# Kernel tuning notes

Hardware: AMD Instinct MI355X
Metric: run time of the kernel (lower is better)

Reference implementation:

```python
import jax, jax.numpy as jnp
import numpy as np

HIDDEN = 256
HEAD = 256
GAMMA = 0.96875
SCALE_BASE = 512  # default scale_base in the standard XPOS module


def xpos_apply(x, offset=0, downscale=False):
    """xpos rotary embedding. x: (B, S, H) with H even."""
    B, S, H = x.shape
    half = H // 2
    dt = x.dtype
    pos = jnp.arange(offset, offset + S, dtype=dt)  # (S,)
    # per-channel xpos scale: ((2i + 0.4H) / (1.4H)) ** (pos / scale_base)
    base_scale = (jnp.arange(0, H, 2, dtype=dt) + 0.4 * H) / (1.4 * H)  # (half,)
    scale = base_scale[None, :] ** (pos[:, None] / SCALE_BASE)          # (S, half)
    if downscale:
        scale = 1.0 / scale
    inv_freq = 1.0 / (10000.0 ** (jnp.arange(half, dtype=dt) / half))   # (half,)
    sinusoid = pos[:, None] * inv_freq[None, :]                         # (S, half)
    sin = jnp.sin(sinusoid) * scale
    cos = jnp.cos(sinusoid) * scale
    # duplicate-interleave columns to width H
    sin2 = jnp.repeat(sin, 2, axis=-1)  # (S, H)
    cos2 = jnp.repeat(cos, 2, axis=-1)
    # rotate_every_two
    x1 = x[..., 0::2]
    x2 = x[..., 1::2]
    rot = jnp.stack([-x2, x1], axis=-1).reshape(x.shape)
    return x * cos2[None] + rot * sin2[None]


def decay_mask(S, dtype):
    n = jnp.arange(S)
    diff = n[:, None] - n[None, :]
    # gamma^(i-j) for i>=j else 0 (clamp exponent to avoid huge values under the mask)
    D = jnp.where(diff >= 0,
                  jnp.asarray(GAMMA, dtype) ** jnp.maximum(diff, 0).astype(dtype),
                  jnp.zeros((), dtype))
    return D


def setup_inputs() -> dict:
    key = jax.random.key(0)
    k1, k2, k3, k4 = jax.random.split(key, 4)
    B, N, S = 2, 8, 2048
    X = jax.random.normal(k1, (B, N, S, HIDDEN), dtype=jnp.float32)
    # kaiming-uniform-ish init: uniform in [-1/sqrt(fan_in), 1/sqrt(fan_in)]
    bound = 1.0 / np.sqrt(HIDDEN)
    W_Q = jax.random.uniform(k2, (HIDDEN, HEAD), jnp.float32, -bound, bound)
    W_K = jax.random.uniform(k3, (HIDDEN, HEAD), jnp.float32, -bound, bound)
    W_V = jax.random.uniform(k4, (HIDDEN, HEAD), jnp.float32, -bound, bound)
    return {"X": X, "W_Q": W_Q, "W_K": W_K, "W_V": W_V}


def reference(X, W_Q, W_K, W_V):
    B, N, S, H = X.shape
    Q = X @ W_Q  # (B, N, S, head)
    K = X @ W_K
    V = X @ W_V
    hd = Q.shape[-1]
    Q = xpos_apply(Q.reshape(B * N, S, hd)).reshape(B, N, S, hd)
    K = xpos_apply(K.reshape(B * N, S, hd), downscale=True).reshape(B, N, S, hd)
    D = decay_mask(S, X.dtype)  # (S, S)
    scores = jnp.einsum('bnsh,bnth->bnst', Q, K) * D  # (B, N, S, S)
    return scores @ V  # (B, N, S, v_dim)
```

## Files before the change

### kernel.cpp

```cpp
#include <hip/hip_runtime.h>
#include <hip/hip_bf16.h>


#define S_LEN 2048
#define HD 256
#define BN 16

typedef _Float16 half8 __attribute__((ext_vector_type(8)));
typedef _Float16 half4 __attribute__((ext_vector_type(4)));
typedef _Float16 half2v __attribute__((ext_vector_type(2)));
typedef float floatx16 __attribute__((ext_vector_type(16)));

__device__ __forceinline__ void gl_lds16(const void* g, void* l) {
  __builtin_amdgcn_global_load_lds(
      (const __attribute__((address_space(1))) unsigned int*)(unsigned long long)g,
      (__attribute__((address_space(3))) unsigned int*)(unsigned int)(unsigned long long)l,
      16, 0, 0);
}

__global__ __launch_bounds__(256) void prep_kernel(
    const float* __restrict__ WQ, const float* __restrict__ WK,
    const float* __restrict__ WV, _Float16* __restrict__ WT,
    _Float16* __restrict__ TBL) {
  const int b = blockIdx.x;
  const int tid = threadIdx.x;
  if (b < 1024) {
    const int idx = b * 256 + tid;
    const int i2 = idx & 127;
    const int pos = idx >> 7;
    float inv_freq = exp2f(-(float)i2 * (13.287712379549449f / 128.0f));
    float lbase = log2f(((float)(2 * i2) + 102.4f) / 358.4f);
    float ang = (float)pos * inv_freq;
    float sn, cs;
    sincosf(ang, &sn, &cs);
    float scl = exp2f((float)pos * (1.0f / 512.0f) * lbase);
    float rscl = 1.0f / scl;
    half2v tq, tk;
    tq[0] = (_Float16)(cs * scl);  tq[1] = (_Float16)(sn * scl);
    tk[0] = (_Float16)(cs * rscl); tk[1] = (_Float16)(sn * rscl);
    *(half2v*)&TBL[(long)idx * 2] = tq;
    *(half2v*)&TBL[(long)(262144 + idx) * 2] = tk;
    return;
  }
  __shared__ _Float16 trans[64][72];
  const int bb = b - 1024;
  const int w = bb >> 4;
  const int tk = ((bb & 15) & 3) * 64;
  const int tn = ((bb & 15) >> 2) * 64;
  const float* W = (w == 0) ? WQ : (w == 1) ? WK : WV;
#pragma unroll
  for (int u = 0; u < 4; ++u) {
    int idx = u * 256 + tid;
    int k = idx >> 4;
    int nq = (idx & 15) * 4;
    float4 v = *(const float4*)&W[(tk + k) * HD + tn + nq];
    trans[nq + 0][k] = (_Float16)v.x;
    trans[nq + 1][k] = (_Float16)v.y;
    trans[nq + 2][k] = (_Float16)v.z;
    trans[nq + 3][k] = (_Float16)v.w;
  }
  __syncthreads();
#pragma unroll
  for (int u = 0; u < 2; ++u) {
    int idx = u * 256 + tid;
    int n = idx >> 3;
    int kq = (idx & 7) * 8;
    *(uint4*)&WT[((long)w * HD + tn + n) * HD + tk + kq] = *(const uint4*)&trans[n][kq];
  }
}

__global__ __launch_bounds__(256) void gemm_qkv_kernel(
    const float* __restrict__ X, const _Float16* __restrict__ WT,
    const _Float16* __restrict__ TBL,
    _Float16* __restrict__ Q, _Float16* __restrict__ K,
    _Float16* __restrict__ VT) {
  __shared__ __align__(16) unsigned char smem[66560];
  unsigned char* ep = smem + 32768;

  const int tid = threadIdx.x;
  const int lane = tid & 63;
  const int w = tid >> 6;
  const int l31 = lane & 31;
  const int lh = lane >> 5;
  const int m0 = blockIdx.x * 64;
  const int mtile = w & 1;
  const int nhalf = w >> 1;

#pragma unroll
  for (int i = 0; i < 8; ++i) {
    int id = i * 256 + tid;
    int row = id >> 5, c = id & 31;
    int p = c ^ (row & 31);
    const float4* s = (const float4*)&X[(long)(m0 + row) * HD + c * 8];
    float4 v0 = s[0], v1 = s[1];
    half8 h;
    h[0] = (_Float16)v0.x; h[1] = (_Float16)v0.y;
    h[2] = (_Float16)v0.z; h[3] = (_Float16)v0.w;
    h[4] = (_Float16)v1.x; h[5] = (_Float16)v1.y;
    h[6] = (_Float16)v1.z; h[7] = (_Float16)v1.w;
    *(half8*)(smem + row * 512 + p * 16) = h;
  }
  __syncthreads();

  const int bn = m0 >> 11;
  const int srow0 = m0 & (S_LEN - 1);
  const int mrow = mtile * 32 + l31;
  const int nbase = nhalf * 128;

  for (int wsel = 0; wsel < 3; ++wsel) {
    const _Float16* Wb = WT + (long)wsel * HD * HD;
    floatx16 acc[4];
#pragma unroll
    for (int nt = 0; nt < 4; ++nt)
#pragma unroll
      for (int e = 0; e < 16; ++e) acc[nt][e] = 0.f;

    half8 b[5][4];
#pragma unroll
    for (int pk = 0; pk < 5; ++pk)
#pragma unroll
      for (int nt = 0; nt < 4; ++nt)
        b[pk][nt] = *(const half8*)(Wb + (long)(nbase + nt * 32 + l31) * HD +
                                    pk * 16 + lh * 8);
#pragma unroll
    for (int ks16 = 0; ks16 < 16; ++ks16) {
      const int slot = ks16 % 5;
      int p = (ks16 * 2 + lh) ^ l31;
      half8 af = *(const half8*)(smem + mrow * 512 + p * 16);
#pragma unroll
      for (int nt = 0; nt < 4; ++nt)
        acc[nt] = __builtin_amdgcn_mfma_f32_32x32x16_f16(af, b[slot][nt], acc[nt], 0, 0, 0);
      if (ks16 + 5 < 16) {
#pragma unroll
        for (int nt = 0; nt < 4; ++nt)
          b[slot][nt] = *(const half8*)(Wb + (long)(nbase + nt * 32 + l31) * HD +
                                        (ks16 + 5) * 16 + lh * 8);
      }
    }

    if (wsel < 2) {
#pragma unroll
      for (int nt = 0; nt < 4; ++nt) {
        int col = nbase + nt * 32 + l31;
#pragma unroll
        for (int reg = 0; reg < 16; ++reg) {
          int rmap = (reg & 3) + 8 * (reg >> 2) + 4 * lh;
          *(_Float16*)(ep + (mtile * 32 + rmap) * 528 + col * 2) =
              (_Float16)acc[nt][reg];
        }
      }
      __syncthreads();
      _Float16* o = wsel ? K : Q;
      const _Float16* tb_base = TBL + (long)wsel * 2048 * 128 * 2;
#pragma unroll
      for (int u = 0; u < 8; ++u) {
        int id = u * 256 + tid;
        int row = id >> 5;
        int cq = (id & 31) * 8;
        half8 x = *(const half8*)(ep + row * 528 + cq * 2);
        half8 t = *(const half8*)&tb_base[((long)(srow0 + row) * 128 + (cq >> 1)) * 2];
        half8 y;
        y[0] = x[0] * t[0] - x[1] * t[1];
        y[1] = x[1] * t[0] + x[0] * t[1];
        y[2] = x[2] * t[2] - x[3] * t[3];
        y[3] = x[3] * t[2] + x[2] * t[3];
        y[4] = x[4] * t[4] - x[5] * t[5];
        y[5] = x[5] * t[4] + x[4] * t[5];
        y[6] = x[6] * t[6] - x[7] * t[7];
        y[7] = x[7] * t[6] + x[6] * t[7];
        *(half8*)&o[(long)(m0 + row) * HD + cq] = y;
      }
      __syncthreads();
    } else {
      __syncthreads();
      _Float16 (*vt)[72] = (_Float16(*)[72])smem;
#pragma unroll
      for (int nt = 0; nt < 4; ++nt) {
        int h = nbase + nt * 32 + l31;
#pragma unroll
        for (int reg = 0; reg < 16; ++reg) {
          int rmap = (reg & 3) + 8 * (reg >> 2) + 4 * lh;
          vt[h][mtile * 32 + rmap] = (_Float16)acc[nt][reg];
        }
      }
      __syncthreads();
#pragma unroll
      for (int u = 0; u < 8; ++u) {
        int id = u * 256 + tid;
        int h = id >> 3, sj = (id & 7) * 8;
        *(uint4*)&VT[((long)bn * HD + h) * S_LEN + srow0 + sj] = *(const uint4*)&vt[h][sj];
      }
    }
  }
}

__global__ __launch_bounds__(256) void retention_kernel(
    const _Float16* __restrict__ Q, const _Float16* __restrict__ K,
    const _Float16* __restrict__ VT, float* __restrict__ out) {
  __shared__ __align__(16) unsigned char smem[74752];
  unsigned char* ksb = smem;
  unsigned char* vsb = smem + 32768;
  _Float16 (*sc)[72] = (_Float16(*)[72])(smem + 65536);

  const int tid = threadIdx.x;
  const int lane = tid & 63;
  const int w = tid >> 6;
  const int l31 = lane & 31;
  const int lh = lane >> 5;
  const int qtile = w >> 1;
  const int ttile = w & 1;
  const int hhalf = w & 1;

  const int L = blockIdx.x;
  const int head = L & 15;
  const int g4 = L >> 4;
  const int qt = (g4 < 16) ? (31 - g4) : (g4 - 16);
  const int q0 = qt * 64;

  const _Float16* Qh = Q + (long)head * S_LEN * HD;
  const _Float16* Kh = K + (long)head * S_LEN * HD;
  const _Float16* VTh = VT + (long)head * HD * S_LEN;

  half8 qf[16];
  {
    const _Float16* qrow = Qh + (long)(q0 + qtile * 32 + l31) * HD + lh * 8;
#pragma unroll
    for (int ks16 = 0; ks16 < 16; ++ks16)
      qf[ks16] = *(const half8*)(qrow + ks16 * 16);
  }

  floatx16 acc[4];
#pragma unroll
  for (int nt = 0; nt < 4; ++nt)
#pragma unroll
    for (int e = 0; e < 16; ++e) acc[nt][e] = 0.f;

  const float LG = -0.0458036896f;
  float Cg[16];
#pragma unroll
  for (int g = 0; g < 4; ++g)
#pragma unroll
    for (int r = 0; r < 4; ++r) Cg[4 * g + r] = exp2f(-(float)(8 * g + r) * LG);

#define STAGE_K(T0)                                                        \
  {                                                                        \
    _Pragma("unroll") for (int j = 0; j < 8; ++j) {                        \
      int li = w * 8 + j;                                                  \
      int row = li * 2 + lh;                                               \
      int c = l31 ^ (row & 31);                                            \
      gl_lds16(Kh + (long)((T0) + row) * HD + c * 8, ksb + li * 1024);     \
    }                                                                      \
  }
#define STAGE_V(T0)                                                        \
  {                                                                        \
    _Pragma("unroll") for (int j = 0; j < 8; ++j) {                        \
      int li = w * 8 + j;                                                  \
      int row = li * 8 + (lane >> 3);                                      \
      int c = (lane & 7) ^ (row & 7);                                      \
      gl_lds16(VTh + (long)row * S_LEN + (T0) + c * 8, vsb + li * 1024);   \
    }                                                                      \
  }

  STAGE_K(0);
  STAGE_V(0);

  for (int kt = 0; kt <= qt; ++kt) {
    const int t0 = kt * 64;
    asm volatile("s_waitcnt vmcnt(0)" ::: "memory");
    __syncthreads();

    floatx16 s;
#pragma unroll
    for (int e = 0; e < 16; ++e) s[e] = 0.f;
    {
      const unsigned char* kbase = ksb + (ttile * 32 + l31) * 512;
#pragma unroll
      for (int ks16 = 0; ks16 < 16; ++ks16) {
        int p = (ks16 * 2 + lh) ^ l31;
        half8 a = *(const half8*)(kbase + p * 16);
        s = __builtin_amdgcn_mfma_f32_32x32x16_f16(a, qf[ks16], s, 0, 0, 0);
      }
    }

    {
      const int qg = q0 + qtile * 32 + l31;
      const int tb = t0 + ttile * 32 + 4 * lh;
      const int dd = qg - tb;
      const float E = exp2f((float)dd * LG);
#pragma unroll
      for (int g = 0; g < 4; ++g) {
        half4 h4;
#pragma unroll
        for (int r = 0; r < 4; ++r) {
          int o = 8 * g + r;
          float wv = (dd >= o) ? E * Cg[4 * g + r] : 0.f;
          h4[r] = (_Float16)(s[4 * g + r] * wv);
        }
        *(half4*)&sc[qtile * 32 + l31][ttile * 32 + 4 * lh + 8 * g] = h4;
      }
    }
    __syncthreads();

    if (kt < qt) STAGE_K(t0 + 64);

#pragma unroll
    for (int kst = 0; kst < 4; ++kst) {
      half8 a = *(const half8*)&sc[qtile * 32 + l31][kst * 16 + lh * 8];
#pragma unroll
      for (int nt = 0; nt < 4; ++nt) {
        int h = hhalf * 128 + nt * 32 + l31;
        int p = (kst * 2 + lh) ^ (h & 7);
        half8 b = *(const half8*)(vsb + h * 128 + p * 16);
        acc[nt] = __builtin_amdgcn_mfma_f32_32x32x16_f16(a, b, acc[nt], 0, 0, 0);
      }
    }
    asm volatile("s_waitcnt vmcnt(0)" ::: "memory");
    __syncthreads();

    if (kt < qt) STAGE_V(t0 + 64);
  }

  const long rbase = (long)head * S_LEN + q0 + qtile * 32;
#pragma unroll
  for (int nt = 0; nt < 4; ++nt) {
    int col = hhalf * 128 + nt * 32 + l31;
#pragma unroll
    for (int reg = 0; reg < 16; ++reg) {
      int rmap = (reg & 3) + 8 * (reg >> 2) + 4 * lh;
      out[(rbase + rmap) * HD + col] = acc[nt][reg];
    }
  }
}

extern "C" void kernel_launch(void* const* d_in, const int* in_sizes, int n_in,
                              void* d_out, int out_size, void* d_ws, size_t ws_size,
                              hipStream_t stream) {
  const float* X  = (const float*)d_in[0];
  const float* WQ = (const float*)d_in[1];
  const float* WK = (const float*)d_in[2];
  const float* WV = (const float*)d_in[3];
  float* out = (float*)d_out;

  _Float16* Qh = (_Float16*)d_ws;
  _Float16* Kh = Qh + (size_t)BN * S_LEN * HD;
  _Float16* VTh = Kh + (size_t)BN * S_LEN * HD;
  _Float16* WT = VTh + (size_t)BN * S_LEN * HD;
  _Float16* TBL = WT + (size_t)3 * HD * HD;

  prep_kernel<<<dim3(1072), dim3(256), 0, stream>>>(WQ, WK, WV, WT, TBL);
  gemm_qkv_kernel<<<dim3((BN * S_LEN) / 64), dim3(256), 0, stream>>>(
      X, WT, TBL, Qh, Kh, VTh);
  retention_kernel<<<dim3(512), dim3(256), 0, stream>>>(Qh, Kh, VTh, out);
}
```

Baseline: 194.5 us.

## Preload V fragments into registers and issue K/V staging together per iteration

Moves all V-tile LDS reads into registers before the score scaling step. That frees the V buffer early enough to issue both the next K and V global-to-LDS loads right after a single barrier, instead of needing a second barrier per iteration before staging V. It also adds launch_bounds(256,2) to cap register use at two blocks per CU. The cost is higher register pressure from holding 16 half8 V fragments per lane, which could cause spills under the tighter bound. A possible race also arises: the sc buffer is read after the barrier while the next iteration's sc writes are guarded only by the top-of-loop barrier.

```diff
diff --git a/kernel.cpp b/kernel.cpp
--- a/kernel.cpp
+++ b/kernel.cpp
@@ -194,7 +194,7 @@
   }
 }
 
-__global__ __launch_bounds__(256) void retention_kernel(
+__global__ __launch_bounds__(256, 2) void retention_kernel(
     const _Float16* __restrict__ Q, const _Float16* __restrict__ K,
     const _Float16* __restrict__ VT, float* __restrict__ out) {
   __shared__ __align__(16) unsigned char smem[74752];
@@ -244,8 +244,8 @@
 
 #define STAGE_K(T0)                                                        \
   {                                                                        \
-    _Pragma("unroll") for (int j = 0; j < 8; ++j) {                        \
-      int li = w * 8 + j;                                                  \
+    _Pragma("unroll") for (int jj = 0; jj < 8; ++jj) {                     \
+      int li = w * 8 + jj;                                                 \
       int row = li * 2 + lh;                                               \
       int c = l31 ^ (row & 31);                                            \
       gl_lds16(Kh + (long)((T0) + row) * HD + c * 8, ksb + li * 1024);     \
@@ -253,8 +253,8 @@
   }
 #define STAGE_V(T0)                                                        \
   {                                                                        \
-    _Pragma("unroll") for (int j = 0; j < 8; ++j) {                        \
-      int li = w * 8 + j;                                                  \
+    _Pragma("unroll") for (int jj = 0; jj < 8; ++jj) {                     \
+      int li = w * 8 + jj;                                                 \
       int row = li * 8 + (lane >> 3);                                      \
       int c = (lane & 7) ^ (row & 7);                                      \
       gl_lds16(VTh + (long)row * S_LEN + (T0) + c * 8, vsb + li * 1024);   \
@@ -281,6 +281,16 @@
         s = __builtin_amdgcn_mfma_f32_32x32x16_f16(a, qf[ks16], s, 0, 0, 0);
       }
     }
+
+    half8 vb[4][4];
+#pragma unroll
+    for (int kst = 0; kst < 4; ++kst)
+#pragma unroll
+      for (int nt = 0; nt < 4; ++nt) {
+        int h = hhalf * 128 + nt * 32 + l31;
+        int p = (kst * 2 + lh) ^ (h & 7);
+        vb[kst][nt] = *(const half8*)(vsb + h * 128 + p * 16);
+      }
 
     {
       const int qg = q0 + qtile * 32 + l31;
@@ -299,25 +309,23 @@
         *(half4*)&sc[qtile * 32 + l31][ttile * 32 + 4 * lh + 8 * g] = h4;
       }
     }
-    __syncthreads();
-
-    if (kt < qt) STAGE_K(t0 + 64);
+
+    asm volatile("s_waitcnt lgkmcnt(0)" ::: "memory");
+    __builtin_amdgcn_s_barrier();
+    __builtin_amdgcn_sched_barrier(0);
+
+    if (kt < qt) {
+      STAGE_K(t0 + 64);
+      STAGE_V(t0 + 64);
+    }
 
 #pragma unroll
     for (int kst = 0; kst < 4; ++kst) {
       half8 a = *(const half8*)&sc[qtile * 32 + l31][kst * 16 + lh * 8];
 #pragma unroll
-      for (int nt = 0; nt < 4; ++nt) {
-        int h = hhalf * 128 + nt * 32 + l31;
-        int p = (kst * 2 + lh) ^ (h & 7);
-        half8 b = *(const half8*)(vsb + h * 128 + p * 16);
-        acc[nt] = __builtin_amdgcn_mfma_f32_32x32x16_f16(a, b, acc[nt], 0, 0, 0);
-      }
-    }
-    asm volatile("s_waitcnt vmcnt(0)" ::: "memory");
-    __syncthreads();
-
-    if (kt < qt) STAGE_V(t0 + 64);
+      for (int nt = 0; nt < 4; ++nt)
+        acc[nt] = __builtin_amdgcn_mfma_f32_32x32x16_f16(a, vb[kst][nt], acc[nt], 0, 0, 0);
+    }
   }
 
   const long rbase = (long)head * S_LEN + q0 + qtile * 32;
```

Result: slower. 272.8 us (+40.2%).
